# Optimization experiments

Hardware: AMD Instinct MI355X
Metric: run time of the kernel (lower is better)

Reference implementation:

```python
import jax, jax.numpy as jnp
import numpy as np

BS, L, DIM, H, POS = 2, 2048, 1024, 16, 16
DH = DIM // H
SCALE = float(np.round(np.sqrt(DH), 2))  # torch code: np.round(np.sqrt(d_head), 2)


def setup_inputs() -> dict:
    key = jax.random.key(0)
    ks = jax.random.split(key, 12)
    init = lambda k, shape: (jax.random.normal(k, shape, dtype=jnp.float32) * 0.02)
    inp = {
        "q": jax.random.normal(ks[0], (BS, L, DIM + POS), dtype=jnp.float32),
        "k": jax.random.normal(ks[1], (BS, L, DIM + POS), dtype=jnp.float32),
        "v": jax.random.normal(ks[2], (BS, L, DIM + POS), dtype=jnp.float32),
        "Wq": init(ks[3], (DIM, DIM)), "bq": jnp.zeros((DIM,), jnp.float32),
        "Wk": init(ks[4], (DIM, DIM)), "bk": jnp.zeros((DIM,), jnp.float32),
        "Wv": init(ks[5], (DIM, DIM)), "bv": jnp.zeros((DIM,), jnp.float32),
        "Wo": init(ks[6], (DIM, DIM)), "bo": jnp.zeros((DIM,), jnp.float32),
        # causal mask: positions with mask==1 are filled with -1e9 (strict upper triangle)
        "attn_mask": jnp.triu(jnp.ones((L, L), jnp.int32), k=1),
        "pos_token_dim": POS,
    }
    return inp


def reference(q, k, v, Wq, bq, Wk, bk, Wv, bv, Wo, bo, attn_mask, pos_token_dim):
    # pos-token suffix: stripped from q/k/v; encoding taken from k's suffix
    encoding = k[..., -pos_token_dim:]                      # [bs, L, pos]
    q = q[..., :-pos_token_dim]
    k = k[..., :-pos_token_dim]
    v = v[..., :-pos_token_dim]
    bs, Ln, dim = q.shape
    h, dh = H, DH

    # QKV projections (torch Linear: x @ W.T + b), split into heads -> [bs, h, L, dh]
    queries = (q @ Wq.T + bq).reshape(bs, Ln, h, dh).transpose(0, 2, 1, 3)
    keys    = (k @ Wk.T + bk).reshape(bs, Ln, h, dh).transpose(0, 2, 1, 3)
    values  = (v @ Wv.T + bv).reshape(bs, Ln, h, dh).transpose(0, 2, 1, 3)

    # full L x L score matrix (faithful to original naive attention)
    scores = jnp.einsum("bhld,bhmd->bhlm", queries, keys) / SCALE
    scores = jnp.where(attn_mask[None, None, :, :] == 1, jnp.float32(-1e9), scores)
    factors = jax.nn.softmax(scores, axis=-1)               # [bs, h, L, L]

    context = jnp.einsum("bhlm,bhmd->bhld", factors, values)
    context = context.transpose(0, 2, 1, 3).reshape(bs, Ln, dim)
    context = context @ Wo.T + bo                           # [bs, L, dim]

    # pos-token passthrough: attend encoding with same factors, mean over heads
    context_encoding = jnp.einsum("bhlm,bmp->bhlp", factors, encoding).mean(axis=1)
    return jnp.concatenate([context, context_encoding], axis=-1)  # [bs, L, dim+pos]
```

## Files before the change

kernel.cpp:

```cpp
#include <hip/hip_runtime.h>
#include <hip/hip_bf16.h>

#define BS   2
#define LEN  2048
#define DIM  1024
#define NH   16
#define DHD  64
#define POSD 16
#define DHE  80
#define NTOK 4096
#define INW  1040

typedef __attribute__((ext_vector_type(8))) short bf16x8;
typedef __attribute__((ext_vector_type(4))) float f32x4;

__device__ __forceinline__ short f2bf(float f) {
    union { float f; unsigned u; } v; v.f = f;
    unsigned r = v.u + 0x7fffu + ((v.u >> 16) & 1u);
    return (short)(r >> 16);
}
__device__ __forceinline__ float bf2f(short s) {
    union { unsigned u; float f; } v; v.u = ((unsigned)(unsigned short)s) << 16;
    return v.f;
}
__device__ __forceinline__ unsigned packbf(float a, float b) {
    union { float f; unsigned u; } x, y; x.f = a; y.f = b;
    return ((x.u + 0x8000u) >> 16) | ((y.u + 0x8000u) & 0xFFFF0000u);
}
__device__ __forceinline__ f32x4 mfma16(bf16x8 a, bf16x8 b, f32x4 c) {
    return __builtin_amdgcn_mfma_f32_16x16x32_bf16(a, b, c, 0, 0, 0);
}
__device__ __forceinline__ void gld16(const short* g, short* l) {
    __builtin_amdgcn_global_load_lds(
        (const __attribute__((address_space(1))) unsigned int*)g,
        (__attribute__((address_space(3))) unsigned int*)l,
        16, 0, 0);
}

__global__ __launch_bounds__(256) void prep_kernel(
    const float* __restrict__ qin, const float* __restrict__ kin, const float* __restrict__ vin,
    const float* __restrict__ Wq, const float* __restrict__ Wk,
    const float* __restrict__ Wv, const float* __restrict__ Wo,
    short* __restrict__ X16, short* __restrict__ W16, short* __restrict__ Vt)
{
    const int NA = 3 * NTOK * DIM / 4;
    const int NW = 4 * DIM * DIM / 4;
    int idx = blockIdx.x * 256 + threadIdx.x;
    if (idx < NA) {
        int per = NTOK * DIM / 4;
        int mi = idx / per, r = idx % per;
        int tok = r >> 8, c4 = r & 255;
        const float* src = (mi == 0 ? qin : (mi == 1 ? kin : vin));
        float4 v = *(const float4*)(src + (size_t)tok * INW + c4 * 4);
        short4 o;
        o.x = f2bf(v.x); o.y = f2bf(v.y); o.z = f2bf(v.z); o.w = f2bf(v.w);
        *(short4*)(X16 + (size_t)mi * NTOK * DIM + (size_t)tok * DIM + c4 * 4) = o;
        return;
    }
    idx -= NA;
    if (idx < NW) {
        int wi = idx >> 18, r = idx & 262143;
        const float* w = (wi == 0 ? Wq : (wi == 1 ? Wk : (wi == 2 ? Wv : Wo)));
        float4 v = *(const float4*)(w + (size_t)r * 4);
        short4 o;
        o.x = f2bf(v.x); o.y = f2bf(v.y); o.z = f2bf(v.z); o.w = f2bf(v.w);
        *(short4*)(W16 + (size_t)wi * DIM * DIM + (size_t)r * 4) = o;
        return;
    }
    idx -= NW;
    if (idx < BS * NH * POSD * (LEN / 8)) {
        int l8 = idx & 255;
        int p  = (idx >> 8) & 15;
        int h  = (idx >> 12) & 15;
        int b  = (idx >> 16);
        int l0 = l8 * 8;
        bf16x8 o;
        for (int i = 0; i < 8; i++)
            o[i] = f2bf(kin[(size_t)(b * LEN + l0 + i) * INW + DIM + p]);
        *(bf16x8*)(Vt + ((size_t)(b * NH + h) * DHE + DHD + p) * LEN + l0) = o;
    }
}

__global__ __launch_bounds__(256) void qkv_gemm(
    const short* __restrict__ X16, const short* __restrict__ W16,
    const float* __restrict__ bq, const float* __restrict__ bk, const float* __restrict__ bv,
    short* __restrict__ Qb, short* __restrict__ Kb, short* __restrict__ Vt)
{
    __shared__ __align__(16) short smem[24576];

    int sw = (blockIdx.x & 7) * 96 + (blockIdx.x >> 3);
    int nt = sw % 24, mt = sw / 24;
    int mat = nt >> 3, ntl = nt & 7;
    const short* A = X16 + (size_t)mat * NTOK * DIM;
    const short* W = W16 + (size_t)mat * DIM * DIM;

    int t = threadIdx.x;
    int w = t >> 6, lane = t & 63, g = lane >> 4, c = lane & 15;
    int wr = w >> 1, wc = w & 1;

    f32x4 acc[4][4];
    #pragma unroll
    for (int i = 0; i < 4; i++)
        #pragma unroll
        for (int j = 0; j < 4; j++)
            acc[i][j] = (f32x4){0.f, 0.f, 0.f, 0.f};

    int row0 = t >> 2, blk0 = t & 3;
    const short* aSrc0 = A + (size_t)(mt * 128 + row0) * DIM + blk0 * 8;
    const short* aSrc1 = aSrc0 + (size_t)64 * DIM;
    const short* bSrc0 = W + (size_t)(ntl * 128 + row0) * DIM + blk0 * 8;
    const short* bSrc1 = bSrc0 + (size_t)64 * DIM;

    short* bufC  = smem;
    short* bufN  = smem + 8192;
    short* bufNN = smem + 16384;

    {
        short* ab = bufC + w * 512;
        gld16(aSrc0, ab);
        gld16(aSrc1, ab + 2048);
        gld16(bSrc0, ab + 4096);
        gld16(bSrc1, ab + 6144);
        ab = bufN + w * 512;
        gld16(aSrc0 + 32, ab);
        gld16(aSrc1 + 32, ab + 2048);
        gld16(bSrc0 + 32, ab + 4096);
        gld16(bSrc1 + 32, ab + 6144);
    }

    for (int k = 0; k < 32; k++) {
        if (k < 30) {
            int k0 = (k + 2) * 32;
            short* ab = bufNN + w * 512;
            gld16(aSrc0 + k0, ab);
            gld16(aSrc1 + k0, ab + 2048);
            gld16(bSrc0 + k0, ab + 4096);
            gld16(bSrc1 + k0, ab + 6144);
            asm volatile("s_waitcnt vmcnt(8)" ::: "memory");
        } else if (k == 30) {
            asm volatile("s_waitcnt vmcnt(4)" ::: "memory");
        } else {
            asm volatile("s_waitcnt vmcnt(0)" ::: "memory");
        }
        __builtin_amdgcn_s_barrier();
        asm volatile("" ::: "memory");

        const short* Asb = bufC;
        const short* Bsb = bufC + 4096;
        bf16x8 af[4], bfr[4];
        #pragma unroll
        for (int fm = 0; fm < 4; fm++)
            af[fm] = *(const bf16x8*)(Asb + (wr * 64 + fm * 16 + c) * 32 + g * 8);
        #pragma unroll
        for (int fn = 0; fn < 4; fn++)
            bfr[fn] = *(const bf16x8*)(Bsb + (wc * 64 + fn * 16 + c) * 32 + g * 8);
        __builtin_amdgcn_s_setprio(1);
        #pragma unroll
        for (int fm = 0; fm < 4; fm++)
            #pragma unroll
            for (int fn = 0; fn < 4; fn++)
                acc[fm][fn] = mfma16(af[fm], bfr[fn], acc[fm][fn]);
        __builtin_amdgcn_s_setprio(0);

        asm volatile("s_waitcnt lgkmcnt(0)" ::: "memory");
        __builtin_amdgcn_s_barrier();
        asm volatile("" ::: "memory");

        short* tmp = bufC; bufC = bufN; bufN = bufNN; bufNN = tmp;
    }

    const float* bias = (mat == 0 ? bq : (mat == 1 ? bk : bv));
    if (mat == 2) {
        __syncthreads();
        #pragma unroll
        for (int fn = 0; fn < 4; fn++) {
            int nl = wc * 64 + fn * 16 + c;
            float bval = bias[ntl * 128 + nl];
            #pragma unroll
            for (int fm = 0; fm < 4; fm++) {
                int m0 = wr * 64 + fm * 16 + g * 4;
                short4 pk;
                pk.x = f2bf(acc[fm][fn][0] + bval);
                pk.y = f2bf(acc[fm][fn][1] + bval);
                pk.z = f2bf(acc[fm][fn][2] + bval);
                pk.w = f2bf(acc[fm][fn][3] + bval);
                *(short4*)(smem + nl * 136 + m0) = pk;
            }
        }
        __syncthreads();
        int b_ = (mt * 128) >> 11;
        int l0 = (mt * 128) & 2047;
        #pragma unroll
        for (int rep = 0; rep < 8; rep++) {
            int idx = rep * 256 + t;
            int row = idx >> 4, ch = idx & 15;
            bf16x8 v = *(const bf16x8*)(smem + row * 136 + ch * 8);
            int ng = ntl * 128 + row, h = ng >> 6, dh = ng & 63;
            *(bf16x8*)(Vt + ((size_t)(b_ * NH + h) * DHE + dh) * LEN + l0 + ch * 8) = v;
        }
    } else {
        float qs = (mat == 0) ? 0.18033688011112042f : 1.0f;
        short* dst = (mat == 0) ? Qb : Kb;
        #pragma unroll
        for (int fn = 0; fn < 4; fn++) {
            int n = ntl * 128 + wc * 64 + fn * 16 + c;
            float bval = bias[n];
            int h = n >> 6, dh = n & 63;
            #pragma unroll
            for (int fm = 0; fm < 4; fm++) {
                int mbase = mt * 128 + wr * 64 + fm * 16 + g * 4;
                #pragma unroll
                for (int i = 0; i < 4; i++) {
                    int m = mbase + i;
                    int b_ = m >> 11, l = m & 2047;
                    dst[((size_t)(b_ * NH + h) * LEN + l) * DHD + dh] =
                        f2bf((acc[fm][fn][i] + bval) * qs);
                }
            }
        }
    }
}

__global__ __launch_bounds__(256, 2) void attn_kernel(
    const short* __restrict__ Qb, const short* __restrict__ Kb,
    const short* __restrict__ Vt, short* __restrict__ Ctx)
{
    __shared__ __align__(16) short Ks[64 * 64];
    __shared__ __align__(16) short Vs[DHE * 64];
    __shared__ __align__(16) short Ps[4][16 * 64];

    int bid = blockIdx.x;
    int u = bid >> 5, bh = bid & 31;
    int qt = (u < 16) ? (2 * u) : (63 - 2 * u);
    int b = bh >> 4, h = bh & 15;
    int q0 = qt * 64;
    int t = threadIdx.x, w = t >> 6, lane = t & 63, g = lane >> 4, c = lane & 15;
    const size_t bhQ = (size_t)(b * NH + h) * LEN;
    const size_t bhV = (size_t)(b * NH + h) * DHE;

    bf16x8 qa0, qa1;
    {
        const short* qp = Qb + (bhQ + q0 + w * 16 + c) * DHD;
        qa0 = *(const bf16x8*)(qp + g * 8);
        qa1 = *(const bf16x8*)(qp + 32 + g * 8);
    }

    int rK = t >> 3, blkS = t & 7;
    int swzS = (blkS ^ (rK & 7)) * 8;
    short* kDst0 = Ks + rK * 64 + swzS;
    short* kDst1 = Ks + (rK + 32) * 64 + swzS;
    short* vDst0 = Vs + rK * 64 + swzS;
    short* vDst1 = Vs + (rK + 32) * 64 + swzS;
    short* vDst2 = Vs + (rK + 64) * 64 + swzS;
    const short* kS0 = Kb + (bhQ + rK) * DHD + blkS * 8;
    const short* kS1 = Kb + (bhQ + rK + 32) * DHD + blkS * 8;
    const short* vS0 = Vt + (bhV + rK) * LEN + blkS * 8;
    const short* vS1 = Vt + (bhV + rK + 32) * LEN + blkS * 8;
    const short* vS2 = Vt + (bhV + rK + 64) * LEN + blkS * 8;
    bool v2on = (t < 128);

    {
        bf16x8 a0 = *(const bf16x8*)kS0;
        bf16x8 a1 = *(const bf16x8*)kS1;
        bf16x8 x0 = *(const bf16x8*)vS0;
        bf16x8 x1 = *(const bf16x8*)vS1;
        bf16x8 x2;
        if (v2on) x2 = *(const bf16x8*)vS2;
        *(bf16x8*)kDst0 = a0;
        *(bf16x8*)kDst1 = a1;
        *(bf16x8*)vDst0 = x0;
        *(bf16x8*)vDst1 = x1;
        if (v2on) *(bf16x8*)vDst2 = x2;
    }
    __syncthreads();

    float lrun = 0.f;
    f32x4 o[5];
    #pragma unroll
    for (int i = 0; i < 5; i++) o[i] = (f32x4){0.f, 0.f, 0.f, 0.f};

    for (int tt = 0; tt <= qt; tt++) {
        bf16x8 kr0, kr1, vr0, vr1, vr2;
        bool pref = (tt < qt);
        if (pref) {
            int kvn = (tt + 1) * 64;
            kr0 = *(const bf16x8*)(kS0 + (size_t)kvn * DHD);
            kr1 = *(const bf16x8*)(kS1 + (size_t)kvn * DHD);
            vr0 = *(const bf16x8*)(vS0 + kvn);
            vr1 = *(const bf16x8*)(vS1 + kvn);
            if (v2on) vr2 = *(const bf16x8*)(vS2 + kvn);
        }

        f32x4 st[4];
        __builtin_amdgcn_s_setprio(1);
        #pragma unroll
        for (int fn = 0; fn < 4; fn++) {
            int row = fn * 16 + c, sw2 = row & 7;
            bf16x8 ka = *(const bf16x8*)(Ks + row * 64 + ((g ^ sw2) * 8));
            bf16x8 kb2 = *(const bf16x8*)(Ks + row * 64 + (((4 + g) ^ sw2) * 8));
            f32x4 z = (f32x4){0.f, 0.f, 0.f, 0.f};
            z = mfma16(ka, qa0, z);
            z = mfma16(kb2, qa1, z);
            st[fn] = z;
        }
        __builtin_amdgcn_s_setprio(0);

        if (tt == qt) {
            #pragma unroll
            for (int fn = 0; fn < 4; fn++)
                #pragma unroll
                for (int i = 0; i < 4; i++)
                    if (fn * 16 + g * 4 + i > w * 16 + c) st[fn][i] = -1e9f;
        }

        float ps = 0.f;
        #pragma unroll
        for (int fn = 0; fn < 4; fn++)
            #pragma unroll
            for (int i = 0; i < 4; i++) {
                float p = __builtin_amdgcn_exp2f(st[fn][i]);
                st[fn][i] = p;
                ps += p;
            }
        ps += __shfl_xor(ps, 16);
        ps += __shfl_xor(ps, 32);
        lrun += ps;

        short* pw = Ps[w];
        #pragma unroll
        for (int fn = 0; fn < 4; fn++) {
            uint2 pu;
            pu.x = packbf(st[fn][0], st[fn][1]);
            pu.y = packbf(st[fn][2], st[fn][3]);
            *(uint2*)(pw + c * 64 + ((((fn << 1) | (g >> 1)) ^ (c & 7)) << 3) + ((g & 1) << 2)) = pu;
        }
        bf16x8 pa0 = *(const bf16x8*)(pw + c * 64 + ((g ^ (c & 7)) * 8));
        bf16x8 pa1 = *(const bf16x8*)(pw + c * 64 + (((4 + g) ^ (c & 7)) * 8));

        __builtin_amdgcn_s_setprio(1);
        #pragma unroll
        for (int fd = 0; fd < 5; fd++) {
            int d = fd * 16 + c, sw2 = d & 7;
            bf16x8 vb0 = *(const bf16x8*)(Vs + d * 64 + ((g ^ sw2) * 8));
            bf16x8 vb1 = *(const bf16x8*)(Vs + d * 64 + (((4 + g) ^ sw2) * 8));
            o[fd] = mfma16(pa0, vb0, o[fd]);
            o[fd] = mfma16(pa1, vb1, o[fd]);
        }
        __builtin_amdgcn_s_setprio(0);

        __syncthreads();
        if (pref) {
            *(bf16x8*)kDst0 = kr0;
            *(bf16x8*)kDst1 = kr1;
            *(bf16x8*)vDst0 = vr0;
            *(bf16x8*)vDst1 = vr1;
            if (v2on) *(bf16x8*)vDst2 = vr2;
        }
        __syncthreads();
    }

    float l0 = __shfl(lrun, g * 4 + 0);
    float l1 = __shfl(lrun, g * 4 + 1);
    float l2 = __shfl(lrun, g * 4 + 2);
    float l3 = __shfl(lrun, g * 4 + 3);
    float inv[4] = {1.f / l0, 1.f / l1, 1.f / l2, 1.f / l3};
    #pragma unroll
    for (int i = 0; i < 4; i++) {
        int q = q0 + w * 16 + g * 4 + i;
        size_t base = (bhQ + q) * DHE;
        #pragma unroll
        for (int fd = 0; fd < 5; fd++)
            Ctx[base + fd * 16 + c] = f2bf(o[fd][i] * inv[i]);
    }
}

__global__ __launch_bounds__(256) void out_gemm(
    const short* __restrict__ Ctx, const short* __restrict__ Wo16,
    const float* __restrict__ bo, float* __restrict__ out)
{
    __shared__ __align__(16) short smem[24576];

    int sw = (blockIdx.x & 7) * 32 + (blockIdx.x >> 3);
    int nt = sw & 7, mt = sw >> 3;
    int t = threadIdx.x;
    int w = t >> 6, lane = t & 63, g = lane >> 4, c = lane & 15;
    int wr = w >> 1, wc = w & 1;

    f32x4 acc[4][4];
    #pragma unroll
    for (int i = 0; i < 4; i++)
        #pragma unroll
        for (int j = 0; j < 4; j++)
            acc[i][j] = (f32x4){0.f, 0.f, 0.f, 0.f};

    int row0 = t >> 2, blk0 = t & 3;
    int tokS = mt * 128 + row0;
    int bS = tokS >> 11, lS = tokS & 2047;
    const short* aBase = Ctx + ((size_t)(bS * NH) * LEN + lS) * DHE + blk0 * 8;
    const short* aBase1 = Ctx + ((size_t)(((tokS + 64) >> 11) * NH) * LEN + ((tokS + 64) & 2047)) * DHE + blk0 * 8;
    const short* bSrc0 = Wo16 + (size_t)(nt * 128 + row0) * DIM + blk0 * 8;
    const short* bSrc1 = bSrc0 + (size_t)64 * DIM;

    short* bufC  = smem;
    short* bufN  = smem + 8192;
    short* bufNN = smem + 16384;

    {
        short* ab = bufC + w * 512;
        gld16(aBase, ab);
        gld16(aBase1, ab + 2048);
        gld16(bSrc0, ab + 4096);
        gld16(bSrc1, ab + 6144);
        ab = bufN + w * 512;
        gld16(aBase + 32, ab);
        gld16(aBase1 + 32, ab + 2048);
        gld16(bSrc0 + 32, ab + 4096);
        gld16(bSrc1 + 32, ab + 6144);
    }

    for (int k = 0; k < 32; k++) {
        if (k < 30) {
            int k0 = (k + 2) * 32;
            size_t aoff = (size_t)(k0 >> 6) * LEN * DHE + (k0 & 63);
            short* ab = bufNN + w * 512;
            gld16(aBase + aoff, ab);
            gld16(aBase1 + aoff, ab + 2048);
            gld16(bSrc0 + k0, ab + 4096);
            gld16(bSrc1 + k0, ab + 6144);
            asm volatile("s_waitcnt vmcnt(8)" ::: "memory");
        } else if (k == 30) {
            asm volatile("s_waitcnt vmcnt(4)" ::: "memory");
        } else {
            asm volatile("s_waitcnt vmcnt(0)" ::: "memory");
        }
        __builtin_amdgcn_s_barrier();
        asm volatile("" ::: "memory");

        const short* Asb = bufC;
        const short* Bsb = bufC + 4096;
        bf16x8 af[4], bfr[4];
        #pragma unroll
        for (int fm = 0; fm < 4; fm++)
            af[fm] = *(const bf16x8*)(Asb + (wr * 64 + fm * 16 + c) * 32 + g * 8);
        #pragma unroll
        for (int fn = 0; fn < 4; fn++)
            bfr[fn] = *(const bf16x8*)(Bsb + (wc * 64 + fn * 16 + c) * 32 + g * 8);
        __builtin_amdgcn_s_setprio(1);
        #pragma unroll
        for (int fm = 0; fm < 4; fm++)
            #pragma unroll
            for (int fn = 0; fn < 4; fn++)
                acc[fm][fn] = mfma16(af[fm], bfr[fn], acc[fm][fn]);
        __builtin_amdgcn_s_setprio(0);

        asm volatile("s_waitcnt lgkmcnt(0)" ::: "memory");
        __builtin_amdgcn_s_barrier();
        asm volatile("" ::: "memory");

        short* tmp = bufC; bufC = bufN; bufN = bufNN; bufNN = tmp;
    }

    #pragma unroll
    for (int fn = 0; fn < 4; fn++) {
        int n = nt * 128 + wc * 64 + fn * 16 + c;
        float bval = bo[n];
        #pragma unroll
        for (int fm = 0; fm < 4; fm++) {
            int mbase = mt * 128 + wr * 64 + fm * 16 + g * 4;
            #pragma unroll
            for (int i = 0; i < 4; i++)
                out[(size_t)(mbase + i) * INW + n] = acc[fm][fn][i] + bval;
        }
    }
}

__global__ __launch_bounds__(256) void encmean_kernel(
    const short* __restrict__ Ctx, float* __restrict__ out)
{
    int idx = blockIdx.x * 256 + threadIdx.x;
    int tok = idx >> 4, p = idx & 15;
    int b = tok >> 11, l = tok & 2047;
    float s = 0.f;
    #pragma unroll
    for (int h = 0; h < NH; h++)
        s += bf2f(Ctx[((size_t)(b * NH + h) * LEN + l) * DHE + DHD + p]);
    out[(size_t)tok * INW + DIM + p] = s * (1.0f / NH);
}

extern "C" void kernel_launch(void* const* d_in, const int* in_sizes, int n_in,
                              void* d_out, int out_size, void* d_ws, size_t ws_size,
                              hipStream_t stream)
{
    const float* qin = (const float*)d_in[0];
    const float* kin = (const float*)d_in[1];
    const float* vin = (const float*)d_in[2];
    const float* Wq  = (const float*)d_in[3];
    const float* bq  = (const float*)d_in[4];
    const float* Wk  = (const float*)d_in[5];
    const float* bk  = (const float*)d_in[6];
    const float* Wv  = (const float*)d_in[7];
    const float* bv  = (const float*)d_in[8];
    const float* Wo  = (const float*)d_in[9];
    const float* bo  = (const float*)d_in[10];
    float* out = (float*)d_out;

    short* X16 = (short*)d_ws;
    short* W16 = X16 + (size_t)3 * NTOK * DIM;
    short* Qb  = W16 + (size_t)4 * DIM * DIM;
    short* Kb  = Qb  + (size_t)NTOK * DIM;
    short* Vt  = Kb  + (size_t)NTOK * DIM;
    short* Ctx = Vt  + (size_t)BS * NH * DHE * LEN;

    prep_kernel<<<16896, 256, 0, stream>>>(qin, kin, vin, Wq, Wk, Wv, Wo, X16, W16, Vt);
    qkv_gemm<<<768, 256, 0, stream>>>(X16, W16, bq, bk, bv, Qb, Kb, Vt);
    attn_kernel<<<1024, 256, 0, stream>>>(Qb, Kb, Vt, Ctx);
    out_gemm<<<256, 256, 0, stream>>>(Ctx, W16 + (size_t)3 * DIM * DIM, bo, out);
    encmean_kernel<<<256, 256, 0, stream>>>(Ctx, out);
}
```

Baseline: 121.5 us.

## Use 8 waves per block in QKV GEMM with smaller per-wave tiles

The QKV projection GEMM goes from 256 to 512 threads per block. The 128x128 output tile is now split across 8 waves arranged 2x4, so each wave computes 64x32 instead of 64x64, and each thread issues half as many global-to-LDS loads per stage. The aim is to raise wave-level parallelism and latency hiding, with launch bounds requesting higher occupancy. In exchange, each wave does fewer MFMAs per LDS fragment read, which lowers register-level reuse of the A fragments.

```diff
diff --git a/kernel.cpp b/kernel.cpp
--- a/kernel.cpp
+++ b/kernel.cpp
@@ -81,7 +81,7 @@
     }
 }
 
-__global__ __launch_bounds__(256) void qkv_gemm(
+__global__ __launch_bounds__(512, 6) void qkv_gemm(
     const short* __restrict__ X16, const short* __restrict__ W16,
     const float* __restrict__ bq, const float* __restrict__ bk, const float* __restrict__ bv,
     short* __restrict__ Qb, short* __restrict__ Kb, short* __restrict__ Vt)
@@ -96,49 +96,35 @@
 
     int t = threadIdx.x;
     int w = t >> 6, lane = t & 63, g = lane >> 4, c = lane & 15;
-    int wr = w >> 1, wc = w & 1;
-
-    f32x4 acc[4][4];
+    int wr = w >> 2, wc = w & 3;
+
+    f32x4 acc[4][2];
     #pragma unroll
     for (int i = 0; i < 4; i++)
         #pragma unroll
-        for (int j = 0; j < 4; j++)
+        for (int j = 0; j < 2; j++)
             acc[i][j] = (f32x4){0.f, 0.f, 0.f, 0.f};
 
-    int row0 = t >> 2, blk0 = t & 3;
-    const short* aSrc0 = A + (size_t)(mt * 128 + row0) * DIM + blk0 * 8;
-    const short* aSrc1 = aSrc0 + (size_t)64 * DIM;
-    const short* bSrc0 = W + (size_t)(ntl * 128 + row0) * DIM + blk0 * 8;
-    const short* bSrc1 = bSrc0 + (size_t)64 * DIM;
+    const short* aSrc = A + (size_t)(mt * 128 + (t >> 2)) * DIM + (t & 3) * 8;
+    const short* bSrc = W + (size_t)(ntl * 128 + (t >> 2)) * DIM + (t & 3) * 8;
 
     short* bufC  = smem;
     short* bufN  = smem + 8192;
     short* bufNN = smem + 16384;
 
-    {
-        short* ab = bufC + w * 512;
-        gld16(aSrc0, ab);
-        gld16(aSrc1, ab + 2048);
-        gld16(bSrc0, ab + 4096);
-        gld16(bSrc1, ab + 6144);
-        ab = bufN + w * 512;
-        gld16(aSrc0 + 32, ab);
-        gld16(aSrc1 + 32, ab + 2048);
-        gld16(bSrc0 + 32, ab + 4096);
-        gld16(bSrc1 + 32, ab + 6144);
-    }
+    gld16(aSrc, bufC + w * 512);
+    gld16(bSrc, bufC + 4096 + w * 512);
+    gld16(aSrc + 32, bufN + w * 512);
+    gld16(bSrc + 32, bufN + 4096 + w * 512);
 
     for (int k = 0; k < 32; k++) {
         if (k < 30) {
             int k0 = (k + 2) * 32;
-            short* ab = bufNN + w * 512;
-            gld16(aSrc0 + k0, ab);
-            gld16(aSrc1 + k0, ab + 2048);
-            gld16(bSrc0 + k0, ab + 4096);
-            gld16(bSrc1 + k0, ab + 6144);
-            asm volatile("s_waitcnt vmcnt(8)" ::: "memory");
+            gld16(aSrc + k0, bufNN + w * 512);
+            gld16(bSrc + k0, bufNN + 4096 + w * 512);
+            asm volatile("s_waitcnt vmcnt(4)" ::: "memory");
         } else if (k == 30) {
-            asm volatile("s_waitcnt vmcnt(4)" ::: "memory");
+            asm volatile("s_waitcnt vmcnt(2)" ::: "memory");
         } else {
             asm volatile("s_waitcnt vmcnt(0)" ::: "memory");
         }
@@ -147,18 +133,18 @@
 
         const short* Asb = bufC;
         const short* Bsb = bufC + 4096;
-        bf16x8 af[4], bfr[4];
+        bf16x8 af[4], bfr[2];
         #pragma unroll
         for (int fm = 0; fm < 4; fm++)
             af[fm] = *(const bf16x8*)(Asb + (wr * 64 + fm * 16 + c) * 32 + g * 8);
         #pragma unroll
-        for (int fn = 0; fn < 4; fn++)
-            bfr[fn] = *(const bf16x8*)(Bsb + (wc * 64 + fn * 16 + c) * 32 + g * 8);
+        for (int fn = 0; fn < 2; fn++)
+            bfr[fn] = *(const bf16x8*)(Bsb + (wc * 32 + fn * 16 + c) * 32 + g * 8);
         __builtin_amdgcn_s_setprio(1);
         #pragma unroll
         for (int fm = 0; fm < 4; fm++)
             #pragma unroll
-            for (int fn = 0; fn < 4; fn++)
+            for (int fn = 0; fn < 2; fn++)
                 acc[fm][fn] = mfma16(af[fm], bfr[fn], acc[fm][fn]);
         __builtin_amdgcn_s_setprio(0);
 
@@ -173,8 +159,8 @@
     if (mat == 2) {
         __syncthreads();
         #pragma unroll
-        for (int fn = 0; fn < 4; fn++) {
-            int nl = wc * 64 + fn * 16 + c;
+        for (int fn = 0; fn < 2; fn++) {
+            int nl = wc * 32 + fn * 16 + c;
             float bval = bias[ntl * 128 + nl];
             #pragma unroll
             for (int fm = 0; fm < 4; fm++) {
@@ -191,8 +177,8 @@
         int b_ = (mt * 128) >> 11;
         int l0 = (mt * 128) & 2047;
         #pragma unroll
-        for (int rep = 0; rep < 8; rep++) {
-            int idx = rep * 256 + t;
+        for (int rep = 0; rep < 4; rep++) {
+            int idx = rep * 512 + t;
             int row = idx >> 4, ch = idx & 15;
             bf16x8 v = *(const bf16x8*)(smem + row * 136 + ch * 8);
             int ng = ntl * 128 + row, h = ng >> 6, dh = ng & 63;
@@ -202,8 +188,8 @@
         float qs = (mat == 0) ? 0.18033688011112042f : 1.0f;
         short* dst = (mat == 0) ? Qb : Kb;
         #pragma unroll
-        for (int fn = 0; fn < 4; fn++) {
-            int n = ntl * 128 + wc * 64 + fn * 16 + c;
+        for (int fn = 0; fn < 2; fn++) {
+            int n = ntl * 128 + wc * 32 + fn * 16 + c;
             float bval = bias[n];
             int h = n >> 6, dh = n & 63;
             #pragma unroll
@@ -512,7 +498,7 @@
     short* Ctx = Vt  + (size_t)BS * NH * DHE * LEN;
 
     prep_kernel<<<16896, 256, 0, stream>>>(qin, kin, vin, Wq, Wk, Wv, Wo, X16, W16, Vt);
-    qkv_gemm<<<768, 256, 0, stream>>>(X16, W16, bq, bk, bv, Qb, Kb, Vt);
+    qkv_gemm<<<768, 512, 0, stream>>>(X16, W16, bq, bk, bv, Qb, Kb, Vt);
     attn_kernel<<<1024, 256, 0, stream>>>(Qb, Kb, Vt, Ctx);
     out_gemm<<<256, 256, 0, stream>>>(Ctx, W16 + (size_t)3 * DIM * DIM, bo, out);
     encmean_kernel<<<256, 256, 0, stream>>>(Ctx, out);
```

Measured after the change: 119.6 us. Within noise of the previous version (-1.6%).
